# Kernel optimization log

Measured on AMD Instinct MI355X. Metric: run time of the kernel, lower is better.

## Reference

```python
import jax, jax.numpy as jnp
import numpy as np

N_HEADS = 32
EPS = 1e-7
ROPE_BASE = 10000.0


def rms_norm(x, gamma):
    return x / jnp.sqrt(EPS + jnp.mean(x * x, axis=-1, keepdims=True)) * gamma


def rope_tables(seq_len, head_dim, dtype=jnp.float32):
    inv_freq = 1.0 / (ROPE_BASE ** (jnp.arange(0, head_dim, 2, dtype=jnp.float32) / head_dim))
    angles = jnp.arange(seq_len, dtype=jnp.float32)[:, None] * inv_freq[None, :]  # [S, D/2]
    angles = jnp.concatenate([angles, angles], axis=-1)  # [S, D]
    return jnp.cos(angles).astype(dtype), jnp.sin(angles).astype(dtype)


def apply_rope(x, cos, sin):
    # x: [B, H, S, D]; cos/sin: [S, D]
    d = x.shape[-1]
    x1, x2 = x[..., : d // 2], x[..., d // 2 :]
    rotated = jnp.concatenate([-x2, x1], axis=-1)
    return x * cos[None, None] + rotated * sin[None, None]


def setup_inputs() -> dict:
    key = jax.random.key(0)
    ks = jax.random.split(key, 9)
    B, S, D, Hd = 1, 2048, 4096, 11008
    s = lambda k, shape, fan: jax.random.normal(k, shape, jnp.float32) * (fan ** -0.5)
    return {
        "X": jax.random.normal(ks[0], (B, S, D), jnp.float32),
        "Wq": s(ks[1], (D, D), D),
        "Wk": s(ks[2], (D, D), D),
        "Wv": s(ks[3], (D, D), D),
        "Wo": s(ks[4], (D, D), D),
        "bo": jnp.zeros((D,), jnp.float32),
        "gamma1": jnp.ones((D,), jnp.float32),
        "gamma2": jnp.ones((D,), jnp.float32),
        "W1": s(ks[5], (D, Hd), D),
        "W2": s(ks[6], (D, Hd), D),
        "W3": s(ks[7], (Hd, D), Hd),
    }


def reference(X, Wq, Wk, Wv, Wo, bo, gamma1, gamma2, W1, W2, W3):
    B, S, D = X.shape
    H = N_HEADS
    hd = D // H

    # --- attention sublayer ---
    h = rms_norm(X, gamma1)
    q = (h @ Wq).reshape(B, S, H, hd).transpose(0, 2, 1, 3)  # [B,H,S,hd]
    k = (h @ Wk).reshape(B, S, H, hd).transpose(0, 2, 1, 3)
    v = (h @ Wv).reshape(B, S, H, hd).transpose(0, 2, 1, 3)

    cos, sin = rope_tables(S, hd, X.dtype)
    q = apply_rope(q, cos, sin)
    k = apply_rope(k, cos, sin)

    scores = jnp.einsum("bhsd,bhtd->bhst", q, k) / jnp.sqrt(jnp.asarray(hd, X.dtype))
    causal = jnp.tril(jnp.ones((S, S), bool))
    scores = jnp.where(causal, scores, -jnp.inf)
    attn = jax.nn.softmax(scores, axis=-1)
    out = jnp.einsum("bhst,bhtd->bhsd", attn, v)
    out = out.transpose(0, 2, 1, 3).reshape(B, S, D)
    out = out @ Wo + bo
    X = X + out

    # --- SwiGLU FFN sublayer ---
    h2 = rms_norm(X, gamma2)
    x1 = h2 @ W1
    x2 = h2 @ W2
    ff = (x1 * jax.nn.sigmoid(x1) * x2) @ W3
    return X + ff
```

## Files before the change

### kernel.cpp

```cpp
#include <hip/hip_runtime.h>
#include <hip/hip_bf16.h>
#include <cstdint>
#include <cmath>

typedef __bf16 bf16;
typedef __attribute__((ext_vector_type(8))) __bf16 bf16x8;
typedef __attribute__((ext_vector_type(4))) __bf16 bf16x4;
typedef __attribute__((ext_vector_type(4))) float f32x4;

__device__ __forceinline__ void gload_lds16(const void* g, void* l) {
  __builtin_amdgcn_global_load_lds((__attribute__((address_space(1))) void*)g,
                                   (__attribute__((address_space(3))) void*)l,
                                   16, 0, 0);
}

template<int BM, int EPI>
__global__ __launch_bounds__(512, 2) void gemmd(
    const bf16* __restrict__ A, const bf16* __restrict__ Bt, void* __restrict__ Cv,
    const float* __restrict__ bias, const float* __restrict__ resid,
    const float* __restrict__ cosT, const float* __restrict__ sinT,
    bf16* __restrict__ q_out, bf16* __restrict__ k_out, bf16* __restrict__ v_out,
    int M, int N, int K, int gm) {
  extern __shared__ char lds[];
  constexpr int ASZ = BM * 128;
  constexpr int BUFS = ASZ + 32768;
  constexpr int MF = BM / 64;
  constexpr int LA = BM / 64;

  const int tid = threadIdx.x;
  const int wave = tid >> 6, lane = tid & 63;
  const int wr = wave >> 1, wc = wave & 1;
  const int l15 = lane & 15, l4 = lane >> 4;
  const int qq = gridDim.x >> 3;
  const int wgid = (blockIdx.x & 7) * qq + (blockIdx.x >> 3);
  const int tm = wgid % gm, tn = wgid / gm;
  const long brow = (long)tm * BM, bcol = (long)tn * 256;
  const int NT = K >> 6;
  const bf16* Ab = A + brow * K;
  const bf16* Bb = Bt + bcol * K;

  f32x4 acc[MF][8];
  #pragma unroll
  for (int i = 0; i < MF; ++i)
    #pragma unroll
    for (int j = 0; j < 8; ++j) acc[i][j] = (f32x4){0.f, 0.f, 0.f, 0.f};

  bf16x8 a[MF][2], b[8][2];

  auto stage = [&](int T) {
    const long kofs = (long)T << 6;
    char* wb = lds + (T & 1) * BUFS;
    #pragma unroll
    for (int i = 0; i < LA; ++i) {
      const int slot = i * 512 + tid, r = slot >> 3, c0 = slot & 7;
      gload_lds16(Ab + (long)r * K + kofs + ((c0 ^ (r & 7)) << 3), wb + slot * 16);
    }
    #pragma unroll
    for (int i = 0; i < 4; ++i) {
      const int slot = i * 512 + tid, r = slot >> 3, c0 = slot & 7;
      gload_lds16(Bb + (long)r * K + kofs + ((c0 ^ (r & 7)) << 3), wb + ASZ + slot * 16);
    }
  };

  stage(0);
  __syncthreads();

  for (int g = 0; g < NT; ++g) {
    const int pg = (g & 1) * BUFS;
    if (g + 1 < NT) stage(g + 1);
    #pragma unroll
    for (int nf = 0; nf < 8; ++nf)
      #pragma unroll
      for (int ks = 0; ks < 2; ++ks) {
        const int r = wc * 128 + nf * 16 + l15;
        b[nf][ks] = *(const bf16x8*)(lds + pg + ASZ + r * 128 + (((ks * 4 + l4) ^ (r & 7)) << 4));
      }
    #pragma unroll
    for (int mf = 0; mf < MF; ++mf)
      #pragma unroll
      for (int ks = 0; ks < 2; ++ks) {
        const int r = wr * (BM / 4) + mf * 16 + l15;
        a[mf][ks] = *(const bf16x8*)(lds + pg + r * 128 + (((ks * 4 + l4) ^ (r & 7)) << 4));
      }
    __builtin_amdgcn_s_setprio(1);
    #pragma unroll
    for (int ks = 0; ks < 2; ++ks)
      #pragma unroll
      for (int mf = 0; mf < MF; ++mf)
        #pragma unroll
        for (int nf = 0; nf < 8; ++nf)
          acc[mf][nf] = __builtin_amdgcn_mfma_f32_16x16x32_bf16(
              a[mf][ks], b[nf][ks], acc[mf][nf], 0, 0, 0);
    __builtin_amdgcn_s_setprio(0);
    __syncthreads();
  }

  if (EPI == 1 || EPI == 2) {
    #pragma unroll
    for (int mf = 0; mf < MF; ++mf) {
      const long row0 = brow + wr * (BM / 4) + mf * 16 + l4 * 4;
      #pragma unroll
      for (int nf = 0; nf < 8; ++nf) {
        const long col = bcol + wc * 128 + nf * 16 + l15;
        #pragma unroll
        for (int rj = 0; rj < 4; ++rj) {
          const long idx = (row0 + rj) * N + col;
          const float v = acc[mf][nf][rj];
          if (EPI == 1) ((float*)Cv)[idx] = v + bias[col] + resid[idx];
          else          ((float*)Cv)[idx] = v + resid[idx];
        }
      }
    }
  } else if (EPI == 3) {
    const int region = (int)(bcol >> 12);
    const int hc = (int)(bcol & 4095) + wc * 128;
    const int h = hc >> 7;
    if (region < 2) {
      bf16* dh = (region == 0 ? q_out : k_out) + (long)h * 2048 * 128;
      #pragma unroll
      for (int mf = 0; mf < MF; ++mf) {
        #pragma unroll
        for (int rj = 0; rj < 4; ++rj) {
          const int s = (int)brow + wr * (BM / 4) + mf * 16 + l4 * 4 + rj;
          const float* cr = cosT + s * 64;
          const float* sr = sinT + s * 64;
          #pragma unroll
          for (int nfp = 0; nfp < 4; ++nfp) {
            const int d = nfp * 16 + l15;
            const float c = cr[d], sn = sr[d];
            const float x1 = acc[mf][nfp][rj], x2 = acc[mf][nfp + 4][rj];
            dh[(long)s * 128 + d]      = (bf16)(x1 * c - x2 * sn);
            dh[(long)s * 128 + d + 64] = (bf16)(x2 * c + x1 * sn);
          }
        }
      }
    } else {
      bf16* dh = v_out + (long)h * 128 * 2048;
      #pragma unroll
      for (int mf = 0; mf < MF; ++mf) {
        const int s0 = (int)brow + wr * (BM / 4) + mf * 16 + l4 * 4;
        #pragma unroll
        for (int nf = 0; nf < 8; ++nf) {
          const int d = nf * 16 + l15;
          bf16x4 v;
          #pragma unroll
          for (int rj = 0; rj < 4; ++rj) v[rj] = (bf16)acc[mf][nf][rj];
          *(bf16x4*)(dh + (long)d * 2048 + s0) = v;
        }
      }
    }
  } else {
    #pragma unroll
    for (int mf = 0; mf < MF; ++mf) {
      #pragma unroll
      for (int rj = 0; rj < 4; ++rj) {
        const int s = (int)brow + wr * (BM / 4) + mf * 16 + l4 * 4 + rj;
        bf16* gr = (bf16*)Cv + (long)s * 11008;
        #pragma unroll
        for (int nfp = 0; nfp < 4; ++nfp) {
          const int col = (int)bcol + wc * 128 + nfp * 32 + l15;
          const int j = ((col >> 5) << 4) + l15;
          const float x1 = acc[mf][2 * nfp][rj], x2 = acc[mf][2 * nfp + 1][rj];
          const float sg = x1 / (1.f + __expf(-x1));
          gr[j] = (bf16)(sg * x2);
        }
      }
    }
  }
}

__global__ __launch_bounds__(256) void rmsnorm_kernel(
    const float* __restrict__ X, const float* __restrict__ gamma,
    bf16* __restrict__ out, int D) {
  const int row = blockIdx.x;
  const float* xr = X + (long)row * D;
  float ss = 0.f;
  for (int i = threadIdx.x * 4; i < D; i += 1024) {
    float4 v = *(const float4*)(xr + i);
    ss += v.x * v.x + v.y * v.y + v.z * v.z + v.w * v.w;
  }
  #pragma unroll
  for (int off = 32; off; off >>= 1) ss += __shfl_down(ss, off, 64);
  __shared__ float wsum[4];
  if ((threadIdx.x & 63) == 0) wsum[threadIdx.x >> 6] = ss;
  __syncthreads();
  const float tot = wsum[0] + wsum[1] + wsum[2] + wsum[3];
  const float scale = rsqrtf(1e-7f + tot / (float)D);
  bf16* orow = out + (long)row * D;
  for (int i = threadIdx.x * 4; i < D; i += 1024) {
    float4 v = *(const float4*)(xr + i);
    float4 g = *(const float4*)(gamma + i);
    orow[i]     = (bf16)(v.x * scale * g.x);
    orow[i + 1] = (bf16)(v.y * scale * g.y);
    orow[i + 2] = (bf16)(v.z * scale * g.z);
    orow[i + 3] = (bf16)(v.w * scale * g.w);
  }
}

__global__ __launch_bounds__(256) void wtrans_kernel(
    const float* __restrict__ in, bf16* __restrict__ out, int R, int C) {
  __shared__ float t[64][65];
  const int bx = blockIdx.x, by = blockIdx.y;
  const int lr = threadIdx.x >> 4;
  const int lc4 = (threadIdx.x & 15) * 4;
  #pragma unroll
  for (int i = 0; i < 4; ++i) {
    const int r = lr + i * 16;
    const float4 v = *(const float4*)(in + (long)(by * 64 + r) * C + bx * 64 + lc4);
    t[r][lc4] = v.x; t[r][lc4 + 1] = v.y; t[r][lc4 + 2] = v.z; t[r][lc4 + 3] = v.w;
  }
  __syncthreads();
  const int oc = threadIdx.x >> 4;
  const int or4 = (threadIdx.x & 15) * 4;
  #pragma unroll
  for (int i = 0; i < 4; ++i) {
    const int c = oc + i * 16;
    bf16x4 v;
    #pragma unroll
    for (int j = 0; j < 4; ++j) v[j] = (bf16)t[or4 + j][c];
    *(bf16x4*)(out + (long)(bx * 64 + c) * R + by * 64 + or4) = v;
  }
}

__global__ __launch_bounds__(256) void w12trans_kernel(
    const float* __restrict__ in, bf16* __restrict__ out, int off) {
  __shared__ float t[64][65];
  const int bx = blockIdx.x, by = blockIdx.y;
  const int lk = threadIdx.x >> 4;
  const int lj4 = (threadIdx.x & 15) * 4;
  #pragma unroll
  for (int i = 0; i < 4; ++i) {
    const int k = lk + i * 16;
    const float4 v = *(const float4*)(in + (long)(by * 64 + k) * 11008 + bx * 64 + lj4);
    t[k][lj4] = v.x; t[k][lj4 + 1] = v.y; t[k][lj4 + 2] = v.z; t[k][lj4 + 3] = v.w;
  }
  __syncthreads();
  const int oj = threadIdx.x >> 4;
  const int ok4 = (threadIdx.x & 15) * 4;
  #pragma unroll
  for (int i = 0; i < 4; ++i) {
    const int j = bx * 64 + oj + i * 16;
    const int r = ((j >> 4) << 5) + off + (j & 15);
    bf16x4 v;
    #pragma unroll
    for (int jj = 0; jj < 4; ++jj) v[jj] = (bf16)t[ok4 + jj][oj + i * 16];
    *(bf16x4*)(out + (long)r * 4096 + by * 64 + ok4) = v;
  }
}

__global__ __launch_bounds__(256) void rope_table_kernel(float* __restrict__ cosT,
                                                         float* __restrict__ sinT) {
  const int idx = blockIdx.x * 256 + threadIdx.x;
  const int i = idx & 63, s = idx >> 6;
  const float inv = powf(10000.f, -(float)i / 64.f);
  const float ang = (float)s * inv;
  cosT[idx] = cosf(ang);
  sinT[idx] = sinf(ang);
}

__global__ __launch_bounds__(256) void attn_kernel(
    const bf16* __restrict__ qh, const bf16* __restrict__ kh,
    const bf16* __restrict__ vt, bf16* __restrict__ outb) {
  constexpr int S = 2048;
  const int qb = blockIdx.x, head = blockIdx.y;
  const int tid = threadIdx.x, wave = tid >> 6, lane = tid & 63;
  __shared__ bf16 Ks[64 * 128];
  __shared__ bf16 Vs[128 * 64];
  __shared__ bf16 Plds[4][16 * 64];
  const bf16* qhh = qh + (long)head * S * 128;
  const bf16* khh = kh + (long)head * S * 128;
  const bf16* vth = vt + (long)head * 128 * S;

  const int l15 = lane & 15, l4 = lane >> 4;
  const int qrow = qb * 64 + wave * 16 + l15;
  bf16x8 qf[4];
  #pragma unroll
  for (int kf = 0; kf < 4; ++kf)
    qf[kf] = *(const bf16x8*)(qhh + (long)qrow * 128 + kf * 32 + l4 * 8);

  float m_r[4], l_r[4];
  #pragma unroll
  for (int r = 0; r < 4; ++r) { m_r[r] = -INFINITY; l_r[r] = 0.f; }
  f32x4 oacc[8] = {};
  const float scale = 0.08838834764831845f;

  for (int tb = 0; tb <= qb; ++tb) {
    #pragma unroll
    for (int i = 0; i < 4; ++i) {
      const int c = wave + 4 * i;
      gload_lds16(khh + (long)(tb * 64 + c * 4 + l4) * 128 + l15 * 8, Ks + c * 512);
      gload_lds16(vth + (long)(c * 8 + (lane >> 3)) * S + tb * 64 + (lane & 7) * 8, Vs + c * 512);
    }
    __syncthreads();

    f32x4 sf[4];
    #pragma unroll
    for (int ft = 0; ft < 4; ++ft) {
      f32x4 acn = {};
      #pragma unroll
      for (int kf = 0; kf < 4; ++kf) {
        bf16x8 kfr = *(const bf16x8*)(Ks + (ft * 16 + l15) * 128 + kf * 32 + l4 * 8);
        acn = __builtin_amdgcn_mfma_f32_16x16x32_bf16(qf[kf], kfr, acn, 0, 0, 0);
      }
      #pragma unroll
      for (int r = 0; r < 4; ++r) sf[ft][r] = acn[r] * scale;
    }
    if (tb == qb) {
      #pragma unroll
      for (int ft = 0; ft < 4; ++ft) {
        const int t_l = ft * 16 + l15;
        #pragma unroll
        for (int r = 0; r < 4; ++r)
          if (t_l > wave * 16 + l4 * 4 + r) sf[ft][r] = -INFINITY;
      }
    }
    float scl[4];
    #pragma unroll
    for (int r = 0; r < 4; ++r) {
      float mx = fmaxf(fmaxf(sf[0][r], sf[1][r]), fmaxf(sf[2][r], sf[3][r]));
      mx = fmaxf(mx, __shfl_xor(mx, 1, 64));
      mx = fmaxf(mx, __shfl_xor(mx, 2, 64));
      mx = fmaxf(mx, __shfl_xor(mx, 4, 64));
      mx = fmaxf(mx, __shfl_xor(mx, 8, 64));
      const float mnew = fmaxf(m_r[r], mx);
      scl[r] = __expf(m_r[r] - mnew);
      m_r[r] = mnew;
      float rs = 0.f;
      #pragma unroll
      for (int ft = 0; ft < 4; ++ft) {
        const float pexp = __expf(sf[ft][r] - mnew);
        sf[ft][r] = pexp;
        rs += pexp;
      }
      rs += __shfl_xor(rs, 1, 64);
      rs += __shfl_xor(rs, 2, 64);
      rs += __shfl_xor(rs, 4, 64);
      rs += __shfl_xor(rs, 8, 64);
      l_r[r] = l_r[r] * scl[r] + rs;
    }
    #pragma unroll
    for (int ft = 0; ft < 4; ++ft)
      #pragma unroll
      for (int r = 0; r < 4; ++r)
        Plds[wave][(l4 * 4 + r) * 64 + ft * 16 + l15] = (bf16)sf[ft][r];
    #pragma unroll
    for (int fd = 0; fd < 8; ++fd)
      #pragma unroll
      for (int r = 0; r < 4; ++r) oacc[fd][r] *= scl[r];
    #pragma unroll
    for (int fd = 0; fd < 8; ++fd) {
      #pragma unroll
      for (int kt = 0; kt < 2; ++kt) {
        bf16x8 pa = *(const bf16x8*)(&Plds[wave][l15 * 64 + kt * 32 + l4 * 8]);
        bf16x8 vb = *(const bf16x8*)(Vs + (fd * 16 + l15) * 64 + kt * 32 + l4 * 8);
        oacc[fd] = __builtin_amdgcn_mfma_f32_16x16x32_bf16(pa, vb, oacc[fd], 0, 0, 0);
      }
    }
    __syncthreads();
  }
  #pragma unroll
  for (int fd = 0; fd < 8; ++fd) {
    #pragma unroll
    for (int r = 0; r < 4; ++r) {
      const long row = qb * 64 + wave * 16 + l4 * 4 + r;
      outb[row * 4096 + head * 128 + fd * 16 + l15] = (bf16)(oacc[fd][r] / l_r[r]);
    }
  }
}

extern "C" void kernel_launch(void* const* d_in, const int* in_sizes, int n_in,
                              void* d_out, int out_size, void* d_ws, size_t ws_size,
                              hipStream_t stream) {
  const float* X  = (const float*)d_in[0];
  const float* Wq = (const float*)d_in[1];
  const float* Wk = (const float*)d_in[2];
  const float* Wv = (const float*)d_in[3];
  const float* Wo = (const float*)d_in[4];
  const float* bo = (const float*)d_in[5];
  const float* g1 = (const float*)d_in[6];
  const float* g2 = (const float*)d_in[7];
  const float* W1 = (const float*)d_in[8];
  const float* W2 = (const float*)d_in[9];
  const float* W3 = (const float*)d_in[10];
  float* out = (float*)d_out;

  hipFuncSetAttribute((const void*)gemmd<256, 3>, hipFuncAttributeMaxDynamicSharedMemorySize, 131072);
  hipFuncSetAttribute((const void*)gemmd<256, 4>, hipFuncAttributeMaxDynamicSharedMemorySize, 131072);
  hipFuncSetAttribute((const void*)gemmd<128, 1>, hipFuncAttributeMaxDynamicSharedMemorySize, 98304);
  hipFuncSetAttribute((const void*)gemmd<128, 2>, hipFuncAttributeMaxDynamicSharedMemorySize, 98304);

  char* p = (char*)d_ws;
  auto alloc = [&](size_t bytes) {
    char* r = p;
    p += (bytes + 255) & ~(size_t)255;
    return r;
  };
  float* cosT = (float*)alloc(2048 * 64 * 4);
  float* sinT = (float*)alloc(2048 * 64 * 4);
  bf16* WqkvT = (bf16*)alloc(12288L * 4096 * 2);
  bf16* WoT  = (bf16*)alloc(4096L * 4096 * 2);
  bf16* W12T = (bf16*)alloc(22016L * 4096 * 2);
  bf16* W3T  = (bf16*)alloc(4096L * 11008 * 2);
  bf16* qhB  = (bf16*)alloc(2048L * 4096 * 2);
  bf16* khB  = (bf16*)alloc(2048L * 4096 * 2);
  bf16* vtB  = (bf16*)alloc(2048L * 4096 * 2);
  bf16* hbuf = (bf16*)alloc(2048L * 4096 * 2);
  bf16* h2   = (bf16*)alloc(2048L * 4096 * 2);
  float* X2  = (float*)alloc(2048L * 4096 * 4);

  bf16* gsw = (bf16*)WqkvT;
  bf16* attnb = hbuf;

  rope_table_kernel<<<512, 256, 0, stream>>>(cosT, sinT);
  wtrans_kernel<<<dim3(64, 64), 256, 0, stream>>>(Wq, WqkvT, 4096, 4096);
  wtrans_kernel<<<dim3(64, 64), 256, 0, stream>>>(Wk, WqkvT + 4096L * 4096, 4096, 4096);
  wtrans_kernel<<<dim3(64, 64), 256, 0, stream>>>(Wv, WqkvT + 2 * 4096L * 4096, 4096, 4096);
  wtrans_kernel<<<dim3(64, 64), 256, 0, stream>>>(Wo, WoT, 4096, 4096);
  w12trans_kernel<<<dim3(172, 64), 256, 0, stream>>>(W1, W12T, 0);
  w12trans_kernel<<<dim3(172, 64), 256, 0, stream>>>(W2, W12T, 16);
  wtrans_kernel<<<dim3(64, 172), 256, 0, stream>>>(W3, W3T, 11008, 4096);

  rmsnorm_kernel<<<2048, 256, 0, stream>>>(X, g1, hbuf, 4096);

  gemmd<256, 3><<<384, 512, 131072, stream>>>(hbuf, WqkvT, nullptr, nullptr, nullptr,
                                              cosT, sinT, qhB, khB, vtB,
                                              2048, 12288, 4096, 8);

  attn_kernel<<<dim3(32, 32), 256, 0, stream>>>(qhB, khB, vtB, attnb);

  gemmd<128, 1><<<256, 512, 98304, stream>>>(attnb, WoT, X2, bo, X,
                                             nullptr, nullptr, nullptr, nullptr, nullptr,
                                             2048, 4096, 4096, 16);

  rmsnorm_kernel<<<2048, 256, 0, stream>>>(X2, g2, h2, 4096);

  gemmd<256, 4><<<688, 512, 131072, stream>>>(h2, W12T, gsw, nullptr, nullptr,
                                              nullptr, nullptr, nullptr, nullptr, nullptr,
                                              2048, 22016, 4096, 8);

  gemmd<128, 2><<<256, 512, 98304, stream>>>(gsw, W3T, out, nullptr, X2,
                                             nullptr, nullptr, nullptr, nullptr, nullptr,
                                             2048, 4096, 11008, 16);
}
```

Baseline: 1.373 ms.

## Shrink GEMM tiles to 128x256xK32 for higher occupancy; double-buffer attention K/V

The GEMM kernel is restructured to a single 128-row tile with a K-step of 32 instead of 64. The LDS layout and swizzle are reworked accordingly, and per-block shared memory drops to 48KB, which allows four workgroups per CU. The QKV and SwiGLU launches double their grid size to match. Separately, the attention kernel double-buffers its K/V tiles so the next block's loads overlap the current block's compute. The risks are that a smaller K-step doubles the barriers per unit of work and 128-row tiles reduce operand reuse.

```diff
diff --git a/kernel.cpp b/kernel.cpp
--- a/kernel.cpp
+++ b/kernel.cpp
@@ -14,18 +14,17 @@
                                    16, 0, 0);
 }
 
-template<int BM, int EPI>
-__global__ __launch_bounds__(512, 2) void gemmd(
+template<int EPI>
+__global__ __launch_bounds__(512, 4) void gemmd(
     const bf16* __restrict__ A, const bf16* __restrict__ Bt, void* __restrict__ Cv,
     const float* __restrict__ bias, const float* __restrict__ resid,
     const float* __restrict__ cosT, const float* __restrict__ sinT,
     bf16* __restrict__ q_out, bf16* __restrict__ k_out, bf16* __restrict__ v_out,
     int M, int N, int K, int gm) {
   extern __shared__ char lds[];
-  constexpr int ASZ = BM * 128;
-  constexpr int BUFS = ASZ + 32768;
-  constexpr int MF = BM / 64;
-  constexpr int LA = BM / 64;
+  constexpr int BM = 128;
+  constexpr int ASZ = BM * 64;
+  constexpr int BUFS = ASZ + 16384;
 
   const int tid = threadIdx.x;
   const int wave = tid >> 6, lane = tid & 63;
@@ -35,30 +34,29 @@
   const int wgid = (blockIdx.x & 7) * qq + (blockIdx.x >> 3);
   const int tm = wgid % gm, tn = wgid / gm;
   const long brow = (long)tm * BM, bcol = (long)tn * 256;
-  const int NT = K >> 6;
+  const int NT = K >> 5;
   const bf16* Ab = A + brow * K;
   const bf16* Bb = Bt + bcol * K;
 
-  f32x4 acc[MF][8];
-  #pragma unroll
-  for (int i = 0; i < MF; ++i)
+  f32x4 acc[2][8];
+  #pragma unroll
+  for (int i = 0; i < 2; ++i)
     #pragma unroll
     for (int j = 0; j < 8; ++j) acc[i][j] = (f32x4){0.f, 0.f, 0.f, 0.f};
 
-  bf16x8 a[MF][2], b[8][2];
-
+  bf16x8 a[2], b[8];
+
+  const int sa_r = tid >> 2, sa_cs = tid & 3;
+  const long aoff = (long)sa_r * K + (((sa_cs - (sa_r >> 1)) & 3) << 3);
   auto stage = [&](int T) {
-    const long kofs = (long)T << 6;
+    const long kofs = (long)T << 5;
     char* wb = lds + (T & 1) * BUFS;
-    #pragma unroll
-    for (int i = 0; i < LA; ++i) {
-      const int slot = i * 512 + tid, r = slot >> 3, c0 = slot & 7;
-      gload_lds16(Ab + (long)r * K + kofs + ((c0 ^ (r & 7)) << 3), wb + slot * 16);
-    }
-    #pragma unroll
-    for (int i = 0; i < 4; ++i) {
-      const int slot = i * 512 + tid, r = slot >> 3, c0 = slot & 7;
-      gload_lds16(Bb + (long)r * K + kofs + ((c0 ^ (r & 7)) << 3), wb + ASZ + slot * 16);
+    gload_lds16(Ab + aoff + kofs, wb + tid * 16);
+    #pragma unroll
+    for (int i = 0; i < 2; ++i) {
+      const int slot = i * 512 + tid, r = slot >> 2, cs = slot & 3;
+      gload_lds16(Bb + (long)r * K + kofs + (((cs - (r >> 1)) & 3) << 3),
+                  wb + ASZ + slot * 16);
     }
   };
 
@@ -69,36 +67,30 @@
     const int pg = (g & 1) * BUFS;
     if (g + 1 < NT) stage(g + 1);
     #pragma unroll
-    for (int nf = 0; nf < 8; ++nf)
-      #pragma unroll
-      for (int ks = 0; ks < 2; ++ks) {
-        const int r = wc * 128 + nf * 16 + l15;
-        b[nf][ks] = *(const bf16x8*)(lds + pg + ASZ + r * 128 + (((ks * 4 + l4) ^ (r & 7)) << 4));
-      }
-    #pragma unroll
-    for (int mf = 0; mf < MF; ++mf)
-      #pragma unroll
-      for (int ks = 0; ks < 2; ++ks) {
-        const int r = wr * (BM / 4) + mf * 16 + l15;
-        a[mf][ks] = *(const bf16x8*)(lds + pg + r * 128 + (((ks * 4 + l4) ^ (r & 7)) << 4));
-      }
+    for (int nf = 0; nf < 8; ++nf) {
+      const int r = wc * 128 + nf * 16 + l15;
+      b[nf] = *(const bf16x8*)(lds + pg + ASZ + r * 64 + (((l4 + (r >> 1)) & 3) << 4));
+    }
+    #pragma unroll
+    for (int mf = 0; mf < 2; ++mf) {
+      const int r = wr * 32 + mf * 16 + l15;
+      a[mf] = *(const bf16x8*)(lds + pg + r * 64 + (((l4 + (r >> 1)) & 3) << 4));
+    }
     __builtin_amdgcn_s_setprio(1);
     #pragma unroll
-    for (int ks = 0; ks < 2; ++ks)
-      #pragma unroll
-      for (int mf = 0; mf < MF; ++mf)
-        #pragma unroll
-        for (int nf = 0; nf < 8; ++nf)
-          acc[mf][nf] = __builtin_amdgcn_mfma_f32_16x16x32_bf16(
-              a[mf][ks], b[nf][ks], acc[mf][nf], 0, 0, 0);
+    for (int mf = 0; mf < 2; ++mf)
+      #pragma unroll
+      for (int nf = 0; nf < 8; ++nf)
+        acc[mf][nf] = __builtin_amdgcn_mfma_f32_16x16x32_bf16(
+            a[mf], b[nf], acc[mf][nf], 0, 0, 0);
     __builtin_amdgcn_s_setprio(0);
     __syncthreads();
   }
 
   if (EPI == 1 || EPI == 2) {
     #pragma unroll
-    for (int mf = 0; mf < MF; ++mf) {
-      const long row0 = brow + wr * (BM / 4) + mf * 16 + l4 * 4;
+    for (int mf = 0; mf < 2; ++mf) {
+      const long row0 = brow + wr * 32 + mf * 16 + l4 * 4;
       #pragma unroll
       for (int nf = 0; nf < 8; ++nf) {
         const long col = bcol + wc * 128 + nf * 16 + l15;
@@ -118,10 +110,10 @@
     if (region < 2) {
       bf16* dh = (region == 0 ? q_out : k_out) + (long)h * 2048 * 128;
       #pragma unroll
-      for (int mf = 0; mf < MF; ++mf) {
+      for (int mf = 0; mf < 2; ++mf) {
         #pragma unroll
         for (int rj = 0; rj < 4; ++rj) {
-          const int s = (int)brow + wr * (BM / 4) + mf * 16 + l4 * 4 + rj;
+          const int s = (int)brow + wr * 32 + mf * 16 + l4 * 4 + rj;
           const float* cr = cosT + s * 64;
           const float* sr = sinT + s * 64;
           #pragma unroll
@@ -137,8 +129,8 @@
     } else {
       bf16* dh = v_out + (long)h * 128 * 2048;
       #pragma unroll
-      for (int mf = 0; mf < MF; ++mf) {
-        const int s0 = (int)brow + wr * (BM / 4) + mf * 16 + l4 * 4;
+      for (int mf = 0; mf < 2; ++mf) {
+        const int s0 = (int)brow + wr * 32 + mf * 16 + l4 * 4;
         #pragma unroll
         for (int nf = 0; nf < 8; ++nf) {
           const int d = nf * 16 + l15;
@@ -151,10 +143,10 @@
     }
   } else {
     #pragma unroll
-    for (int mf = 0; mf < MF; ++mf) {
+    for (int mf = 0; mf < 2; ++mf) {
       #pragma unroll
       for (int rj = 0; rj < 4; ++rj) {
-        const int s = (int)brow + wr * (BM / 4) + mf * 16 + l4 * 4 + rj;
+        const int s = (int)brow + wr * 32 + mf * 16 + l4 * 4 + rj;
         bf16* gr = (bf16*)Cv + (long)s * 11008;
         #pragma unroll
         for (int nfp = 0; nfp < 4; ++nfp) {
@@ -264,8 +256,8 @@
   constexpr int S = 2048;
   const int qb = blockIdx.x, head = blockIdx.y;
   const int tid = threadIdx.x, wave = tid >> 6, lane = tid & 63;
-  __shared__ bf16 Ks[64 * 128];
-  __shared__ bf16 Vs[128 * 64];
+  __shared__ bf16 Ks[2][64 * 128];
+  __shared__ bf16 Vs[2][128 * 64];
   __shared__ bf16 Plds[4][16 * 64];
   const bf16* qhh = qh + (long)head * S * 128;
   const bf16* khh = kh + (long)head * S * 128;
@@ -278,20 +270,27 @@
   for (int kf = 0; kf < 4; ++kf)
     qf[kf] = *(const bf16x8*)(qhh + (long)qrow * 128 + kf * 32 + l4 * 8);
 
+  auto stageKV = [&](int tb, int buf) {
+    #pragma unroll
+    for (int i = 0; i < 4; ++i) {
+      const int c = wave + 4 * i;
+      gload_lds16(khh + (long)(tb * 64 + c * 4 + l4) * 128 + l15 * 8, Ks[buf] + c * 512);
+      gload_lds16(vth + (long)(c * 8 + (lane >> 3)) * S + tb * 64 + (lane & 7) * 8, Vs[buf] + c * 512);
+    }
+  };
+
   float m_r[4], l_r[4];
   #pragma unroll
   for (int r = 0; r < 4; ++r) { m_r[r] = -INFINITY; l_r[r] = 0.f; }
   f32x4 oacc[8] = {};
   const float scale = 0.08838834764831845f;
 
+  stageKV(0, 0);
+  __syncthreads();
+
   for (int tb = 0; tb <= qb; ++tb) {
-    #pragma unroll
-    for (int i = 0; i < 4; ++i) {
-      const int c = wave + 4 * i;
-      gload_lds16(khh + (long)(tb * 64 + c * 4 + l4) * 128 + l15 * 8, Ks + c * 512);
-      gload_lds16(vth + (long)(c * 8 + (lane >> 3)) * S + tb * 64 + (lane & 7) * 8, Vs + c * 512);
-    }
-    __syncthreads();
+    const int buf = tb & 1;
+    if (tb < qb) stageKV(tb + 1, buf ^ 1);
 
     f32x4 sf[4];
     #pragma unroll
@@ -299,7 +298,7 @@
       f32x4 acn = {};
       #pragma unroll
       for (int kf = 0; kf < 4; ++kf) {
-        bf16x8 kfr = *(const bf16x8*)(Ks + (ft * 16 + l15) * 128 + kf * 32 + l4 * 8);
+        bf16x8 kfr = *(const bf16x8*)(Ks[buf] + (ft * 16 + l15) * 128 + kf * 32 + l4 * 8);
         acn = __builtin_amdgcn_mfma_f32_16x16x32_bf16(qf[kf], kfr, acn, 0, 0, 0);
       }
       #pragma unroll
@@ -352,7 +351,7 @@
       #pragma unroll
       for (int kt = 0; kt < 2; ++kt) {
         bf16x8 pa = *(const bf16x8*)(&Plds[wave][l15 * 64 + kt * 32 + l4 * 8]);
-        bf16x8 vb = *(const bf16x8*)(Vs + (fd * 16 + l15) * 64 + kt * 32 + l4 * 8);
+        bf16x8 vb = *(const bf16x8*)(Vs[buf] + (fd * 16 + l15) * 64 + kt * 32 + l4 * 8);
         oacc[fd] = __builtin_amdgcn_mfma_f32_16x16x32_bf16(pa, vb, oacc[fd], 0, 0, 0);
       }
     }
@@ -384,10 +383,10 @@
   const float* W3 = (const float*)d_in[10];
   float* out = (float*)d_out;
 
-  hipFuncSetAttribute((const void*)gemmd<256, 3>, hipFuncAttributeMaxDynamicSharedMemorySize, 131072);
-  hipFuncSetAttribute((const void*)gemmd<256, 4>, hipFuncAttributeMaxDynamicSharedMemorySize, 131072);
-  hipFuncSetAttribute((const void*)gemmd<128, 1>, hipFuncAttributeMaxDynamicSharedMemorySize, 98304);
-  hipFuncSetAttribute((const void*)gemmd<128, 2>, hipFuncAttributeMaxDynamicSharedMemorySize, 98304);
+  hipFuncSetAttribute((const void*)gemmd<1>, hipFuncAttributeMaxDynamicSharedMemorySize, 49152);
+  hipFuncSetAttribute((const void*)gemmd<2>, hipFuncAttributeMaxDynamicSharedMemorySize, 49152);
+  hipFuncSetAttribute((const void*)gemmd<3>, hipFuncAttributeMaxDynamicSharedMemorySize, 49152);
+  hipFuncSetAttribute((const void*)gemmd<4>, hipFuncAttributeMaxDynamicSharedMemorySize, 49152);
 
   char* p = (char*)d_ws;
   auto alloc = [&](size_t bytes) {
@@ -422,23 +421,23 @@
 
   rmsnorm_kernel<<<2048, 256, 0, stream>>>(X, g1, hbuf, 4096);
 
-  gemmd<256, 3><<<384, 512, 131072, stream>>>(hbuf, WqkvT, nullptr, nullptr, nullptr,
-                                              cosT, sinT, qhB, khB, vtB,
-                                              2048, 12288, 4096, 8);
+  gemmd<3><<<768, 512, 49152, stream>>>(hbuf, WqkvT, nullptr, nullptr, nullptr,
+                                        cosT, sinT, qhB, khB, vtB,
+                                        2048, 12288, 4096, 16);
 
   attn_kernel<<<dim3(32, 32), 256, 0, stream>>>(qhB, khB, vtB, attnb);
 
-  gemmd<128, 1><<<256, 512, 98304, stream>>>(attnb, WoT, X2, bo, X,
-                                             nullptr, nullptr, nullptr, nullptr, nullptr,
-                                             2048, 4096, 4096, 16);
+  gemmd<1><<<256, 512, 49152, stream>>>(attnb, WoT, X2, bo, X,
+                                        nullptr, nullptr, nullptr, nullptr, nullptr,
+                                        2048, 4096, 4096, 16);
 
   rmsnorm_kernel<<<2048, 256, 0, stream>>>(X2, g2, h2, 4096);
 
-  gemmd<256, 4><<<688, 512, 131072, stream>>>(h2, W12T, gsw, nullptr, nullptr,
-                                              nullptr, nullptr, nullptr, nullptr, nullptr,
-                                              2048, 22016, 4096, 8);
-
-  gemmd<128, 2><<<256, 512, 98304, stream>>>(gsw, W3T, out, nullptr, X2,
-                                             nullptr, nullptr, nullptr, nullptr, nullptr,
-                                             2048, 4096, 11008, 16);
-}
+  gemmd<4><<<1376, 512, 49152, stream>>>(h2, W12T, gsw, nullptr, nullptr,
+                                         nullptr, nullptr, nullptr, nullptr, nullptr,
+                                         2048, 22016, 4096, 16);
+
+  gemmd<2><<<256, 512, 49152, stream>>>(gsw, W3T, out, nullptr, X2,
+                                        nullptr, nullptr, nullptr, nullptr, nullptr,
+                                        2048, 4096, 11008, 16);
+}
```

New measurement: 1.567 ms. 1.14x slower.

## Add 8-wave interleaved-staging SwiGLU GEMM and double-buffer K/V in attention

Applied to the files above, without the earlier changes.

Replaces the W1/W2 SwiGLU GEMM with a dedicated kernel that splits each K tile into halves. It issues global-to-LDS loads for upcoming tiles between the MFMA quarter-blocks, using explicit barriers and vmcnt waits, so memory traffic overlaps with matrix math. The attention kernel now double-buffers K and V tiles in LDS, prefetching the next tile while computing on the current one, which removes one barrier per iteration. This costs more LDS in attention, which may lower occupancy, and adds fragile hand-tuned synchronisation in the GEMM.

```diff
diff --git a/kernel.cpp b/kernel.cpp
--- a/kernel.cpp
+++ b/kernel.cpp
@@ -12,6 +12,128 @@
   __builtin_amdgcn_global_load_lds((__attribute__((address_space(1))) void*)g,
                                    (__attribute__((address_space(3))) void*)l,
                                    16, 0, 0);
+}
+
+#define BARX __builtin_amdgcn_s_barrier()
+#define LGKM0 asm volatile("s_waitcnt lgkmcnt(0)" ::: "memory")
+#define PRIO1 __builtin_amdgcn_s_setprio(1)
+#define PRIO0 __builtin_amdgcn_s_setprio(0)
+
+__global__ __launch_bounds__(512, 2) void gemm8_sw(
+    const bf16* __restrict__ A, const bf16* __restrict__ Bt,
+    bf16* __restrict__ gout, int M, int N, int K, int gm) {
+  extern __shared__ char lds[];
+  const int tid = threadIdx.x;
+  const int wave = tid >> 6, lane = tid & 63;
+  const int wr = wave >> 2, wc = wave & 3;
+  const int l15 = lane & 15, l4 = lane >> 4;
+  const int qq = gridDim.x >> 3;
+  const int wgid = (blockIdx.x & 7) * qq + (blockIdx.x >> 3);
+  const int tm = wgid % gm, tn = wgid / gm;
+  const long brow = (long)tm * 256, bcol = (long)tn * 256;
+  const int NT = K >> 6;
+  const bf16* Ab = A + brow * K;
+  const bf16* Bb = Bt + bcol * K;
+
+  f32x4 acc[8][4];
+  #pragma unroll
+  for (int i = 0; i < 8; ++i)
+    #pragma unroll
+    for (int j = 0; j < 4; ++j) acc[i][j] = (f32x4){0.f, 0.f, 0.f, 0.f};
+
+  bf16x8 a[4][2], b[4][2];
+
+  auto stage_half = [&](int T, int isB, int half) {
+    const bf16* src = (isB ? Bb : Ab) + (long)(half * 128) * K + ((long)T << 6);
+    char* dst = lds + (T & 1) * 65536 + isB * 32768 + half * 16384;
+    #pragma unroll
+    for (int i = 0; i < 2; ++i) {
+      const int slot = i * 512 + tid, r = slot >> 3, c = slot & 7;
+      gload_lds16(src + (long)r * K + ((c ^ (r & 7)) << 3), dst + slot * 16);
+    }
+  };
+  auto lda = [&](int buf, int mh) {
+    #pragma unroll
+    for (int mf = 0; mf < 4; ++mf) {
+      const int rr = mh * 64 + mf * 16 + l15;
+      const char* base = lds + buf * 65536 + wr * 16384 + rr * 128;
+      #pragma unroll
+      for (int ks = 0; ks < 2; ++ks)
+        a[mf][ks] = *(const bf16x8*)(base + (((ks * 4 + l4) ^ (rr & 7)) << 4));
+    }
+  };
+  auto ldb = [&](int buf) {
+    #pragma unroll
+    for (int nf = 0; nf < 4; ++nf) {
+      const int rr = (wc & 1) * 64 + nf * 16 + l15;
+      const char* base = lds + buf * 65536 + 32768 + (wc >> 1) * 16384 + rr * 128;
+      #pragma unroll
+      for (int ks = 0; ks < 2; ++ks)
+        b[nf][ks] = *(const bf16x8*)(base + (((ks * 4 + l4) ^ (rr & 7)) << 4));
+    }
+  };
+
+  #define QMFMA(MH, NH) do {                                                   \
+    _Pragma("unroll") for (int ks = 0; ks < 2; ++ks)                            \
+    _Pragma("unroll") for (int mf = 0; mf < 4; ++mf)                            \
+    _Pragma("unroll") for (int nf = 0; nf < 2; ++nf)                            \
+      acc[(MH)*4+mf][(NH)*2+nf] = __builtin_amdgcn_mfma_f32_16x16x32_bf16(      \
+          a[mf][ks], b[(NH)*2+nf][ks], acc[(MH)*4+mf][(NH)*2+nf], 0, 0, 0);     \
+  } while (0)
+
+  stage_half(0, 0, 0); stage_half(0, 0, 1); stage_half(0, 1, 0); stage_half(0, 1, 1);
+  stage_half(1, 1, 0); stage_half(1, 1, 1); stage_half(1, 0, 0);
+  asm volatile("s_waitcnt vmcnt(6)" ::: "memory");
+  BARX;
+
+  const int NI = NT >> 1;
+  for (int j = 0; j < NI; ++j) {
+    const int t0 = 2 * j;
+    const bool s = (t0 + 2 < NT);
+    lda(0, 0); ldb(0);
+    stage_half(t0 + 1, 0, 1);
+    BARX; PRIO1; QMFMA(0, 0); PRIO0; LGKM0; BARX;
+    if (s) stage_half(t0 + 2, 1, 0);
+    BARX; PRIO1; QMFMA(0, 1); PRIO0; BARX;
+    lda(0, 1);
+    if (s) stage_half(t0 + 2, 1, 1);
+    BARX; PRIO1; QMFMA(1, 0); PRIO0; LGKM0; BARX;
+    if (s) stage_half(t0 + 2, 0, 0);
+    BARX; PRIO1; QMFMA(1, 1); PRIO0;
+    if (s) asm volatile("s_waitcnt vmcnt(6)" ::: "memory");
+    else   asm volatile("s_waitcnt vmcnt(0)" ::: "memory");
+    BARX;
+    lda(1, 0); ldb(1);
+    if (s) stage_half(t0 + 2, 0, 1);
+    BARX; PRIO1; QMFMA(0, 0); PRIO0; LGKM0; BARX;
+    if (s) stage_half(t0 + 3, 1, 0);
+    BARX; PRIO1; QMFMA(0, 1); PRIO0; BARX;
+    lda(1, 1);
+    if (s) stage_half(t0 + 3, 1, 1);
+    BARX; PRIO1; QMFMA(1, 0); PRIO0; LGKM0; BARX;
+    if (s) stage_half(t0 + 3, 0, 0);
+    BARX; PRIO1; QMFMA(1, 1); PRIO0;
+    if (s) asm volatile("s_waitcnt vmcnt(6)" ::: "memory");
+    BARX;
+  }
+  #undef QMFMA
+
+  #pragma unroll
+  for (int mf = 0; mf < 8; ++mf) {
+    #pragma unroll
+    for (int rj = 0; rj < 4; ++rj) {
+      const int sA = (int)brow + wr * 128 + mf * 16 + l4 * 4 + rj;
+      bf16* gr = gout + (long)sA * 11008;
+      #pragma unroll
+      for (int q = 0; q < 2; ++q) {
+        const int col = (int)bcol + wc * 64 + q * 32 + l15;
+        const int jj = ((col >> 5) << 4) + l15;
+        const float x1 = acc[mf][2 * q][rj], x2 = acc[mf][2 * q + 1][rj];
+        const float sg = x1 / (1.f + __expf(-x1));
+        gr[jj] = (bf16)(sg * x2);
+      }
+    }
+  }
 }
 
 template<int BM, int EPI>
@@ -82,7 +204,7 @@
         const int r = wr * (BM / 4) + mf * 16 + l15;
         a[mf][ks] = *(const bf16x8*)(lds + pg + r * 128 + (((ks * 4 + l4) ^ (r & 7)) << 4));
       }
-    __builtin_amdgcn_s_setprio(1);
+    PRIO1;
     #pragma unroll
     for (int ks = 0; ks < 2; ++ks)
       #pragma unroll
@@ -91,7 +213,7 @@
         for (int nf = 0; nf < 8; ++nf)
           acc[mf][nf] = __builtin_amdgcn_mfma_f32_16x16x32_bf16(
               a[mf][ks], b[nf][ks], acc[mf][nf], 0, 0, 0);
-    __builtin_amdgcn_s_setprio(0);
+    PRIO0;
     __syncthreads();
   }
 
@@ -149,23 +271,6 @@
         }
       }
     }
-  } else {
-    #pragma unroll
-    for (int mf = 0; mf < MF; ++mf) {
-      #pragma unroll
-      for (int rj = 0; rj < 4; ++rj) {
-        const int s = (int)brow + wr * (BM / 4) + mf * 16 + l4 * 4 + rj;
-        bf16* gr = (bf16*)Cv + (long)s * 11008;
-        #pragma unroll
-        for (int nfp = 0; nfp < 4; ++nfp) {
-          const int col = (int)bcol + wc * 128 + nfp * 32 + l15;
-          const int j = ((col >> 5) << 4) + l15;
-          const float x1 = acc[mf][2 * nfp][rj], x2 = acc[mf][2 * nfp + 1][rj];
-          const float sg = x1 / (1.f + __expf(-x1));
-          gr[j] = (bf16)(sg * x2);
-        }
-      }
-    }
   }
 }
 
@@ -264,8 +369,8 @@
   constexpr int S = 2048;
   const int qb = blockIdx.x, head = blockIdx.y;
   const int tid = threadIdx.x, wave = tid >> 6, lane = tid & 63;
-  __shared__ bf16 Ks[64 * 128];
-  __shared__ bf16 Vs[128 * 64];
+  __shared__ bf16 Ks[2][64 * 128];
+  __shared__ bf16 Vs[2][128 * 64];
   __shared__ bf16 Plds[4][16 * 64];
   const bf16* qhh = qh + (long)head * S * 128;
   const bf16* khh = kh + (long)head * S * 128;
@@ -278,20 +383,27 @@
   for (int kf = 0; kf < 4; ++kf)
     qf[kf] = *(const bf16x8*)(qhh + (long)qrow * 128 + kf * 32 + l4 * 8);
 
+  auto stageKV = [&](int tb, int buf) {
+    #pragma unroll
+    for (int i = 0; i < 4; ++i) {
+      const int c = wave + 4 * i;
+      gload_lds16(khh + (long)(tb * 64 + c * 4 + l4) * 128 + l15 * 8, Ks[buf] + c * 512);
+      gload_lds16(vth + (long)(c * 8 + (lane >> 3)) * S + tb * 64 + (lane & 7) * 8, Vs[buf] + c * 512);
+    }
+  };
+
   float m_r[4], l_r[4];
   #pragma unroll
   for (int r = 0; r < 4; ++r) { m_r[r] = -INFINITY; l_r[r] = 0.f; }
   f32x4 oacc[8] = {};
   const float scale = 0.08838834764831845f;
 
+  stageKV(0, 0);
+  __syncthreads();
+
   for (int tb = 0; tb <= qb; ++tb) {
-    #pragma unroll
-    for (int i = 0; i < 4; ++i) {
-      const int c = wave + 4 * i;
-      gload_lds16(khh + (long)(tb * 64 + c * 4 + l4) * 128 + l15 * 8, Ks + c * 512);
-      gload_lds16(vth + (long)(c * 8 + (lane >> 3)) * S + tb * 64 + (lane & 7) * 8, Vs + c * 512);
-    }
-    __syncthreads();
+    const int buf = tb & 1;
+    if (tb < qb) stageKV(tb + 1, buf ^ 1);
 
     f32x4 sf[4];
     #pragma unroll
@@ -299,7 +411,7 @@
       f32x4 acn = {};
       #pragma unroll
       for (int kf = 0; kf < 4; ++kf) {
-        bf16x8 kfr = *(const bf16x8*)(Ks + (ft * 16 + l15) * 128 + kf * 32 + l4 * 8);
+        bf16x8 kfr = *(const bf16x8*)(Ks[buf] + (ft * 16 + l15) * 128 + kf * 32 + l4 * 8);
         acn = __builtin_amdgcn_mfma_f32_16x16x32_bf16(qf[kf], kfr, acn, 0, 0, 0);
       }
       #pragma unroll
@@ -352,7 +464,7 @@
       #pragma unroll
       for (int kt = 0; kt < 2; ++kt) {
         bf16x8 pa = *(const bf16x8*)(&Plds[wave][l15 * 64 + kt * 32 + l4 * 8]);
-        bf16x8 vb = *(const bf16x8*)(Vs + (fd * 16 + l15) * 64 + kt * 32 + l4 * 8);
+        bf16x8 vb = *(const bf16x8*)(Vs[buf] + (fd * 16 + l15) * 64 + kt * 32 + l4 * 8);
         oacc[fd] = __builtin_amdgcn_mfma_f32_16x16x32_bf16(pa, vb, oacc[fd], 0, 0, 0);
       }
     }
@@ -385,7 +497,7 @@
   float* out = (float*)d_out;
 
   hipFuncSetAttribute((const void*)gemmd<256, 3>, hipFuncAttributeMaxDynamicSharedMemorySize, 131072);
-  hipFuncSetAttribute((const void*)gemmd<256, 4>, hipFuncAttributeMaxDynamicSharedMemorySize, 131072);
+  hipFuncSetAttribute((const void*)gemm8_sw, hipFuncAttributeMaxDynamicSharedMemorySize, 131072);
   hipFuncSetAttribute((const void*)gemmd<128, 1>, hipFuncAttributeMaxDynamicSharedMemorySize, 98304);
   hipFuncSetAttribute((const void*)gemmd<128, 2>, hipFuncAttributeMaxDynamicSharedMemorySize, 98304);
 
@@ -434,9 +546,7 @@
 
   rmsnorm_kernel<<<2048, 256, 0, stream>>>(X2, g2, h2, 4096);
 
-  gemmd<256, 4><<<688, 512, 131072, stream>>>(h2, W12T, gsw, nullptr, nullptr,
-                                              nullptr, nullptr, nullptr, nullptr, nullptr,
-                                              2048, 22016, 4096, 8);
+  gemm8_sw<<<688, 512, 131072, stream>>>(h2, W12T, gsw, 2048, 22016, 4096, 8);
 
   gemmd<128, 2><<<256, 512, 98304, stream>>>(gsw, W3T, out, nullptr, X2,
                                              nullptr, nullptr, nullptr, nullptr, nullptr,
```

New measurement: 1.381 ms. Within noise of the previous version (+0.6%).
